# Kernel tuning notes

Measured on AMD Instinct MI355X. Metric: run time of the kernel, lower is better.

Reference implementation:

```python
import jax, jax.numpy as jnp
import numpy as np

WS = 7          # window size (square)
NUM_HEADS = 4
DIM = 128
B_ = 16384
NW = 64         # number of distinct shift masks


def _relative_coords(ws):
    # [N, N, 2] normalized relative coordinates, N = ws*ws
    ch = jnp.arange(ws, dtype=jnp.float32)
    cw = jnp.arange(ws, dtype=jnp.float32)
    coords = jnp.stack(jnp.meshgrid(ch, cw, indexing='ij'))          # [2, ws, ws]
    flat = coords.reshape(2, -1)                                      # [2, N]
    rel = flat[:, :, None] - flat[:, None, :]                         # [2, N, N]
    rel = jnp.transpose(rel, (1, 2, 0))                               # [N, N, 2]
    denom = jnp.array([max(ws - 1, 1), max(ws - 1, 1)], jnp.float32)
    return rel / denom


def setup_inputs() -> dict:
    key = jax.random.key(0)
    ks = jax.random.split(key, 8)
    N = WS * WS
    return {
        'x': jax.random.normal(ks[0], (B_, N, DIM), jnp.float32),
        'mask': jax.random.normal(ks[1], (NW, N, N), jnp.float32),
        'qkv_w': jax.random.normal(ks[2], (DIM, 3 * DIM), jnp.float32) * 0.02,
        'qkv_b': jnp.zeros((3 * DIM,), jnp.float32),
        'mlp_w1': jax.random.normal(ks[3], (2, 64), jnp.float32) * 0.5,
        'mlp_b1': jnp.zeros((64,), jnp.float32),
        'mlp_w2': jax.random.normal(ks[4], (64, NUM_HEADS), jnp.float32) * 0.1,
        'mlp_b2': jnp.zeros((NUM_HEADS,), jnp.float32),
        'proj_w': jax.random.normal(ks[5], (DIM, DIM), jnp.float32) * 0.02,
        'proj_b': jnp.zeros((DIM,), jnp.float32),
    }


def reference(x, mask, qkv_w, qkv_b, mlp_w1, mlp_b1, mlp_w2, mlp_b2, proj_w, proj_b):
    B, N, C = x.shape
    H = NUM_HEADS
    hd = C // H
    scale = hd ** (-0.5)

    qkv = (x @ qkv_w + qkv_b).reshape(B, N, 3, H, hd)
    qkv = jnp.transpose(qkv, (2, 0, 3, 1, 4))          # [3, B, H, N, hd]
    q, k, v = qkv[0] * scale, qkv[1], qkv[2]

    attn = jnp.einsum('bhnd,bhmd->bhnm', q, k)          # [B, H, N, N]

    # MLP-derived relative position bias (exact-erf GELU, as torch nn.GELU default)
    rel = _relative_coords(WS)                          # [N, N, 2]
    hmid = jax.nn.gelu(rel @ mlp_w1 + mlp_b1, approximate=False)
    bias = hmid @ mlp_w2 + mlp_b2                       # [N, N, H]
    bias = jnp.transpose(bias, (2, 0, 1))               # [H, N, N]
    attn = attn + bias[None]

    nW = mask.shape[0]
    attn = attn.reshape(B // nW, nW, H, N, N) + mask[None, :, None]
    attn = attn.reshape(B, H, N, N)
    attn = jax.nn.softmax(attn, axis=-1)

    out = jnp.einsum('bhnm,bhmd->bhnd', attn, v)        # [B, H, N, hd]
    out = jnp.transpose(out, (0, 2, 1, 3)).reshape(B, N, C)
    return out @ proj_w + proj_b
```

## Files before the change

kernel.cpp:

```cpp
#include <hip/hip_runtime.h>
#include <hip/hip_bf16.h>
#include <math.h>

typedef __bf16 bf16_t;
typedef __bf16 bf16x4 __attribute__((ext_vector_type(4)));
typedef __bf16 bf16x8 __attribute__((ext_vector_type(8)));
typedef float  f32x4  __attribute__((ext_vector_type(4)));

#define QKV_SCALE 0.17677669529663687f

#define WS_QKVWT   0u
#define WS_PROJWT  98304u
#define WS_QKVB    131072u
#define WS_BM      135168u

__global__ __launch_bounds__(256) void prep_kernel(
    const float* __restrict__ mask,
    const float* __restrict__ qkv_w, const float* __restrict__ qkv_b,
    const float* __restrict__ mlp_w1, const float* __restrict__ mlp_b1,
    const float* __restrict__ mlp_w2, const float* __restrict__ mlp_b2,
    const float* __restrict__ proj_w,
    bf16_t* __restrict__ qkv_wT, bf16_t* __restrict__ proj_wT,
    float* __restrict__ qkv_bs, float* __restrict__ bm)
{
    const int blk = blockIdx.x;
    const int tid = threadIdx.x;
    if (blk < 16) {
        const int cell = blk * 256 + tid;
        const int q = cell >> 6, kk = cell & 63;
        if (q < 49 && kk < 49) {
            const float dy = (float)(q / 7 - kk / 7) * (1.0f / 6.0f);
            const float dx = (float)(q % 7 - kk % 7) * (1.0f / 6.0f);
            float b0 = mlp_b2[0], b1 = mlp_b2[1], b2 = mlp_b2[2], b3 = mlp_b2[3];
            for (int j = 0; j < 64; ++j) {
                const float pre = dy * mlp_w1[j] + dx * mlp_w1[64 + j] + mlp_b1[j];
                const float g = 0.5f * pre * (1.0f + erff(pre * 0.70710678118654752f));
                b0 += g * mlp_w2[j * 4 + 0];
                b1 += g * mlp_w2[j * 4 + 1];
                b2 += g * mlp_w2[j * 4 + 2];
                b3 += g * mlp_w2[j * 4 + 3];
            }
            const int nm = q * 49 + kk;
            for (int wi = 0; wi < 64; ++wi) {
                const float mv = mask[wi * 2401 + nm];
                bm[(size_t)((wi * 4 + 0) << 12) + cell] = mv + b0;
                bm[(size_t)((wi * 4 + 1) << 12) + cell] = mv + b1;
                bm[(size_t)((wi * 4 + 2) << 12) + cell] = mv + b2;
                bm[(size_t)((wi * 4 + 3) << 12) + cell] = mv + b3;
            }
        } else {
            const float val = (kk >= 49) ? -3.0e38f : 0.0f;
            for (int t = 0; t < 256; ++t)
                bm[(size_t)(t << 12) + cell] = val;
        }
    } else if (blk < 208) {
        const int idx = (blk - 16) * 256 + tid;
        const int n = idx >> 7, k = idx & 127;
        float v = qkv_w[k * 384 + n];
        if (n < 128) v *= QKV_SCALE;
        qkv_wT[idx] = (bf16_t)v;
    } else if (blk < 272) {
        const int idx = (blk - 208) * 256 + tid;
        const int n = idx >> 7, k = idx & 127;
        proj_wT[idx] = (bf16_t)proj_w[k * 128 + n];
    } else {
        if (tid < 384) {
            float v = qkv_b[tid];
            if (tid < 128) v *= QKV_SCALE;
            qkv_bs[tid] = v;
        }
    }
}

__global__ __launch_bounds__(256, 3) void swin_main_kernel(
    const float* __restrict__ x,
    const bf16_t* __restrict__ qkv_wT,
    const bf16_t* __restrict__ proj_wT,
    const float* __restrict__ qkv_bs,
    const float* __restrict__ proj_b,
    const float* __restrict__ bm,
    float* __restrict__ out)
{
    __shared__ __align__(16) unsigned char smem[49152];

    const int b    = blockIdx.x;
    const int tid  = threadIdx.x;
    const int w    = tid >> 6;
    const int lane = tid & 63;
    const int c16  = lane & 15;
    const int q4   = lane >> 4;
    const int WB   = w * 12288;
    const int VB   = WB + 8192;
    const int swz  = (c16 & 7) << 4;
    const float* xg = x + (size_t)b * 6272;

    const f32x4 zf = {0.f, 0.f, 0.f, 0.f};

    f32x4 qk[4][4];
    f32x4 va[4][2];
#pragma unroll
    for (int mt = 0; mt < 4; ++mt) {
#pragma unroll
        for (int nt = 0; nt < 4; ++nt) qk[mt][nt] = zf;
        va[mt][0] = zf; va[mt][1] = zf;
    }
    const int colQK[4] = {32 * w, 32 * w + 16, 128 + 32 * w, 128 + 32 * w + 16};
    bool tv[4];
#pragma unroll
    for (int nt = 0; nt < 4; ++nt) tv[nt] = (c16 + 16 * nt) < 49;

#pragma unroll
    for (int ks = 0; ks < 4; ++ks) {
        bf16x8 xf[4];
#pragma unroll
        for (int nt = 0; nt < 4; ++nt) {
            if (tv[nt]) {
                const float* p = xg + (c16 + 16 * nt) * 128 + ks * 32 + q4 * 8;
                float4 a0 = *(const float4*)p;
                float4 a1 = *(const float4*)(p + 4);
                xf[nt][0] = (bf16_t)a0.x; xf[nt][1] = (bf16_t)a0.y;
                xf[nt][2] = (bf16_t)a0.z; xf[nt][3] = (bf16_t)a0.w;
                xf[nt][4] = (bf16_t)a1.x; xf[nt][5] = (bf16_t)a1.y;
                xf[nt][6] = (bf16_t)a1.z; xf[nt][7] = (bf16_t)a1.w;
            } else {
#pragma unroll
                for (int j = 0; j < 8; ++j) xf[nt][j] = (bf16_t)0.0f;
            }
        }
#pragma unroll
        for (int mt = 0; mt < 4; ++mt) {
            const bf16x8 wf = *(const bf16x8*)(qkv_wT + (colQK[mt] + c16) * 128 + ks * 32 + q4 * 8);
#pragma unroll
            for (int nt = 0; nt < 4; ++nt)
                qk[mt][nt] = __builtin_amdgcn_mfma_f32_16x16x32_bf16(wf, xf[nt], qk[mt][nt], 0, 0, 0);
        }
#pragma unroll
        for (int nt = 0; nt < 2; ++nt) {
            const bf16x8 vf = *(const bf16x8*)(qkv_wT + (256 + 32 * w + 16 * nt + c16) * 128 + ks * 32 + q4 * 8);
#pragma unroll
            for (int mt = 0; mt < 4; ++mt)
                va[mt][nt] = __builtin_amdgcn_mfma_f32_16x16x32_bf16(xf[mt], vf, va[mt][nt], 0, 0, 0);
        }
    }

#pragma unroll
    for (int mt = 0; mt < 4; ++mt) {
        const float4 qb = *(const float4*)(qkv_bs + colQK[mt] + 4 * q4);
        const int dim0 = (mt < 2 ? 16 * mt : 32 + 16 * (mt - 2)) + 4 * q4;
#pragma unroll
        for (int nt = 0; nt < 4; ++nt) {
            const int tok = c16 + 16 * nt;
            bf16x4 pk;
            pk[0] = (bf16_t)(qk[mt][nt][0] + qb.x);
            pk[1] = (bf16_t)(qk[mt][nt][1] + qb.y);
            pk[2] = (bf16_t)(qk[mt][nt][2] + qb.z);
            pk[3] = (bf16_t)(qk[mt][nt][3] + qb.w);
            *(bf16x4*)&smem[(WB + tok * 128 + dim0 * 2) ^ swz] = pk;
        }
    }
#pragma unroll
    for (int nt = 0; nt < 2; ++nt) {
        const float qv = qkv_bs[256 + 32 * w + 16 * nt + c16];
        const int dim = c16 + 16 * nt;
#pragma unroll
        for (int mt = 0; mt < 4; ++mt) {
            const int tok0 = 16 * mt + 4 * q4;
            bf16x4 pk;
            pk[0] = (bf16_t)(va[mt][nt][0] + qv);
            pk[1] = (bf16_t)(va[mt][nt][1] + qv);
            pk[2] = (bf16_t)(va[mt][nt][2] + qv);
            pk[3] = (bf16_t)(va[mt][nt][3] + qv);
            *(bf16x4*)&smem[(VB + dim * 128 + tok0 * 2) ^ swz] = pk;
        }
    }

    f32x4 st[4][4];
    {
        bf16x8 ka[4], qb_[4];
#pragma unroll
        for (int mt = 0; mt < 4; ++mt)
            ka[mt] = *(const bf16x8*)&smem[(WB + (c16 + 16 * mt) * 128 + 64 + 16 * q4) ^ swz];
#pragma unroll
        for (int nt = 0; nt < 4; ++nt)
            qb_[nt] = *(const bf16x8*)&smem[(WB + (c16 + 16 * nt) * 128 + 16 * q4) ^ swz];
#pragma unroll
        for (int mt = 0; mt < 4; ++mt)
#pragma unroll
            for (int nt = 0; nt < 4; ++nt)
                st[mt][nt] = __builtin_amdgcn_mfma_f32_16x16x32_bf16(ka[mt], qb_[nt], zf, 0, 0, 0),
                st[mt][nt] = st[mt][nt];
    }

    const float* bq = bm + ((size_t)(((b & 63) << 2) + w) << 12);
#pragma unroll
    for (int nt = 0; nt < 4; ++nt) {
        const int q = c16 + 16 * nt;
        float4 bv[4];
#pragma unroll
        for (int mt = 0; mt < 4; ++mt)
            bv[mt] = *(const float4*)(bq + q * 64 + 16 * mt + 4 * q4);
        float mx = -3.0e38f;
#pragma unroll
        for (int mt = 0; mt < 4; ++mt) {
            st[mt][nt][0] += bv[mt].x; st[mt][nt][1] += bv[mt].y;
            st[mt][nt][2] += bv[mt].z; st[mt][nt][3] += bv[mt].w;
#pragma unroll
            for (int r = 0; r < 4; ++r) mx = fmaxf(mx, st[mt][nt][r]);
        }
        mx = fmaxf(mx, __shfl_xor(mx, 16));
        mx = fmaxf(mx, __shfl_xor(mx, 32));
        float sm = 0.0f;
#pragma unroll
        for (int mt = 0; mt < 4; ++mt)
#pragma unroll
            for (int r = 0; r < 4; ++r) {
                const float p = __expf(st[mt][nt][r] - mx);
                st[mt][nt][r] = p;
                sm += p;
            }
        sm += __shfl_xor(sm, 16);
        sm += __shfl_xor(sm, 32);
        const float rp = 1.0f / sm;
#pragma unroll
        for (int mt = 0; mt < 4; ++mt) {
            bf16x4 pk;
#pragma unroll
            for (int r = 0; r < 4; ++r) pk[r] = (bf16_t)(st[mt][nt][r] * rp);
            *(bf16x4*)&smem[(WB + q * 128 + (16 * mt + 4 * q4) * 2) ^ swz] = pk;
        }
    }

    f32x4 ot[2][4];
#pragma unroll
    for (int mt = 0; mt < 2; ++mt)
#pragma unroll
        for (int nt = 0; nt < 4; ++nt) ot[mt][nt] = zf;
#pragma unroll
    for (int ksv = 0; ksv < 2; ++ksv) {
        bf16x8 av[2], bp[4];
#pragma unroll
        for (int mt = 0; mt < 2; ++mt)
            av[mt] = *(const bf16x8*)&smem[(VB + (c16 + 16 * mt) * 128 + 64 * ksv + 16 * q4) ^ swz];
#pragma unroll
        for (int nt = 0; nt < 4; ++nt)
            bp[nt] = *(const bf16x8*)&smem[(WB + (c16 + 16 * nt) * 128 + 64 * ksv + 16 * q4) ^ swz];
#pragma unroll
        for (int mt = 0; mt < 2; ++mt)
#pragma unroll
            for (int nt = 0; nt < 4; ++nt)
                ot[mt][nt] = __builtin_amdgcn_mfma_f32_16x16x32_bf16(av[mt], bp[nt], ot[mt][nt], 0, 0, 0);
    }

    __syncthreads();

#pragma unroll
    for (int mt = 0; mt < 2; ++mt)
#pragma unroll
        for (int nt = 0; nt < 4; ++nt) {
            const int q = c16 + 16 * nt;
            bf16x4 pk;
#pragma unroll
            for (int r = 0; r < 4; ++r) pk[r] = (bf16_t)ot[mt][nt][r];
            *(bf16x4*)&smem[(q * 256 + (32 * w + 16 * mt + 4 * q4) * 2) ^ swz] = pk;
        }
    __syncthreads();

    f32x4 pj[2][4];
#pragma unroll
    for (int mt = 0; mt < 2; ++mt)
#pragma unroll
        for (int nt = 0; nt < 4; ++nt) pj[mt][nt] = zf;
#pragma unroll
    for (int ks = 0; ks < 4; ++ks) {
        bf16x8 aw[2], bo[4];
#pragma unroll
        for (int mt = 0; mt < 2; ++mt)
            aw[mt] = *(const bf16x8*)(proj_wT + (32 * w + 16 * mt + c16) * 128 + ks * 32 + q4 * 8);
#pragma unroll
        for (int nt = 0; nt < 4; ++nt)
            bo[nt] = *(const bf16x8*)&smem[((c16 + 16 * nt) * 256 + 64 * ks + 16 * q4) ^ swz];
#pragma unroll
        for (int mt = 0; mt < 2; ++mt)
#pragma unroll
            for (int nt = 0; nt < 4; ++nt)
                pj[mt][nt] = __builtin_amdgcn_mfma_f32_16x16x32_bf16(aw[mt], bo[nt], pj[mt][nt], 0, 0, 0);
    }

    float* og = out + (size_t)b * 6272;
#pragma unroll
    for (int mt = 0; mt < 2; ++mt) {
        const int oc0 = 32 * w + 16 * mt + 4 * q4;
        const float4 pb = *(const float4*)(proj_b + oc0);
#pragma unroll
        for (int nt = 0; nt < 4; ++nt) {
            const int tok = c16 + 16 * nt;
            if (tok < 49) {
                float4 v;
                v.x = pj[mt][nt][0] + pb.x;
                v.y = pj[mt][nt][1] + pb.y;
                v.z = pj[mt][nt][2] + pb.z;
                v.w = pj[mt][nt][3] + pb.w;
                *(float4*)(og + tok * 128 + oc0) = v;
            }
        }
    }
}

extern "C" void kernel_launch(void* const* d_in, const int* in_sizes, int n_in,
                              void* d_out, int out_size, void* d_ws, size_t ws_size,
                              hipStream_t stream) {
    const float* x      = (const float*)d_in[0];
    const float* mask   = (const float*)d_in[1];
    const float* qkv_w  = (const float*)d_in[2];
    const float* qkv_b  = (const float*)d_in[3];
    const float* mlp_w1 = (const float*)d_in[4];
    const float* mlp_b1 = (const float*)d_in[5];
    const float* mlp_w2 = (const float*)d_in[6];
    const float* mlp_b2 = (const float*)d_in[7];
    const float* proj_w = (const float*)d_in[8];
    const float* proj_b = (const float*)d_in[9];
    float* out = (float*)d_out;

    unsigned char* ws = (unsigned char*)d_ws;
    bf16_t* qkv_wT  = (bf16_t*)(ws + WS_QKVWT);
    bf16_t* proj_wT = (bf16_t*)(ws + WS_PROJWT);
    float*  qkv_bs  = (float*)(ws + WS_QKVB);
    float*  bm      = (float*)(ws + WS_BM);

    hipLaunchKernelGGL(prep_kernel, dim3(273), dim3(256), 0, stream,
                       mask, qkv_w, qkv_b, mlp_w1, mlp_b1, mlp_w2, mlp_b2, proj_w,
                       qkv_wT, proj_wT, qkv_bs, bm);
    hipLaunchKernelGGL(swin_main_kernel, dim3(16384), dim3(256), 0, stream,
                       x, qkv_wT, proj_wT, qkv_bs, proj_b, bm, out);
}
```

Before: 718.6 us.

## Keep Q/K/V and softmax probabilities in registers, shrink LDS to 16KB

Q, K, V and the softmax probabilities are now repacked directly from the MFMA accumulator layout into bf16x8 operand fragments, so they no longer round-trip through shared memory. Only the per-head attention output still goes through LDS before the projection. LDS shrinks from 48KB to 16KB, and occupancy is pinned to 4 waves per EU instead of the old launch-bound hint. Projection weights are loaded with interleaved output channels so each thread writes two contiguous float4s. The V GEMM is split into a separate pass that reloads x, which adds global/L2 traffic and register pressure in exchange for removing LDS traffic.

```diff
diff --git a/kernel.cpp b/kernel.cpp
--- a/kernel.cpp
+++ b/kernel.cpp
@@ -72,7 +72,8 @@
     }
 }
 
-__global__ __launch_bounds__(256, 3) void swin_main_kernel(
+__global__ __launch_bounds__(256) __attribute__((amdgpu_waves_per_eu(4, 4)))
+void swin_main_kernel(
     const float* __restrict__ x,
     const bf16_t* __restrict__ qkv_wT,
     const bf16_t* __restrict__ proj_wT,
@@ -81,7 +82,7 @@
     const float* __restrict__ bm,
     float* __restrict__ out)
 {
-    __shared__ __align__(16) unsigned char smem[49152];
+    __shared__ __align__(16) unsigned char smem[16384];
 
     const int b    = blockIdx.x;
     const int tid  = threadIdx.x;
@@ -89,25 +90,21 @@
     const int lane = tid & 63;
     const int c16  = lane & 15;
     const int q4   = lane >> 4;
-    const int WB   = w * 12288;
-    const int VB   = WB + 8192;
     const int swz  = (c16 & 7) << 4;
     const float* xg = x + (size_t)b * 6272;
-
     const f32x4 zf = {0.f, 0.f, 0.f, 0.f};
 
+    bool tv[4];
+#pragma unroll
+    for (int nt = 0; nt < 4; ++nt) tv[nt] = (c16 + 16 * nt) < 49;
+
+    const int colQK[4] = {32 * w, 32 * w + 16, 128 + 32 * w, 128 + 32 * w + 16};
+
     f32x4 qk[4][4];
-    f32x4 va[4][2];
-#pragma unroll
-    for (int mt = 0; mt < 4; ++mt) {
+#pragma unroll
+    for (int mt = 0; mt < 4; ++mt)
 #pragma unroll
         for (int nt = 0; nt < 4; ++nt) qk[mt][nt] = zf;
-        va[mt][0] = zf; va[mt][1] = zf;
-    }
-    const int colQK[4] = {32 * w, 32 * w + 16, 128 + 32 * w, 128 + 32 * w + 16};
-    bool tv[4];
-#pragma unroll
-    for (int nt = 0; nt < 4; ++nt) tv[nt] = (c16 + 16 * nt) < 49;
 
 #pragma unroll
     for (int ks = 0; ks < 4; ++ks) {
@@ -134,67 +131,84 @@
             for (int nt = 0; nt < 4; ++nt)
                 qk[mt][nt] = __builtin_amdgcn_mfma_f32_16x16x32_bf16(wf, xf[nt], qk[mt][nt], 0, 0, 0);
         }
-#pragma unroll
-        for (int nt = 0; nt < 2; ++nt) {
-            const bf16x8 vf = *(const bf16x8*)(qkv_wT + (256 + 32 * w + 16 * nt + c16) * 128 + ks * 32 + q4 * 8);
+    }
+
+    bf16x8 Qf[4], Kf[4];
+    {
+        const float4 b0 = *(const float4*)(qkv_bs + colQK[0] + 4 * q4);
+        const float4 b1 = *(const float4*)(qkv_bs + colQK[1] + 4 * q4);
+        const float4 b2 = *(const float4*)(qkv_bs + colQK[2] + 4 * q4);
+        const float4 b3 = *(const float4*)(qkv_bs + colQK[3] + 4 * q4);
+#pragma unroll
+        for (int nt = 0; nt < 4; ++nt) {
+            Qf[nt][0] = (bf16_t)(qk[0][nt][0] + b0.x); Qf[nt][1] = (bf16_t)(qk[0][nt][1] + b0.y);
+            Qf[nt][2] = (bf16_t)(qk[0][nt][2] + b0.z); Qf[nt][3] = (bf16_t)(qk[0][nt][3] + b0.w);
+            Qf[nt][4] = (bf16_t)(qk[1][nt][0] + b1.x); Qf[nt][5] = (bf16_t)(qk[1][nt][1] + b1.y);
+            Qf[nt][6] = (bf16_t)(qk[1][nt][2] + b1.z); Qf[nt][7] = (bf16_t)(qk[1][nt][3] + b1.w);
+            Kf[nt][0] = (bf16_t)(qk[2][nt][0] + b2.x); Kf[nt][1] = (bf16_t)(qk[2][nt][1] + b2.y);
+            Kf[nt][2] = (bf16_t)(qk[2][nt][2] + b2.z); Kf[nt][3] = (bf16_t)(qk[2][nt][3] + b2.w);
+            Kf[nt][4] = (bf16_t)(qk[3][nt][0] + b3.x); Kf[nt][5] = (bf16_t)(qk[3][nt][1] + b3.y);
+            Kf[nt][6] = (bf16_t)(qk[3][nt][2] + b3.z); Kf[nt][7] = (bf16_t)(qk[3][nt][3] + b3.w);
+        }
+    }
+
+    f32x4 va[4][2];
+#pragma unroll
+    for (int mt = 0; mt < 4; ++mt) { va[mt][0] = zf; va[mt][1] = zf; }
+
+#pragma unroll
+    for (int ks = 0; ks < 4; ++ks) {
+        bf16x8 xf[4];
+#pragma unroll
+        for (int nt = 0; nt < 4; ++nt) {
+            if (tv[nt]) {
+                const float* p = xg + (c16 + 16 * nt) * 128 + ks * 32 + q4 * 8;
+                float4 a0 = *(const float4*)p;
+                float4 a1 = *(const float4*)(p + 4);
+                xf[nt][0] = (bf16_t)a0.x; xf[nt][1] = (bf16_t)a0.y;
+                xf[nt][2] = (bf16_t)a0.z; xf[nt][3] = (bf16_t)a0.w;
+                xf[nt][4] = (bf16_t)a1.x; xf[nt][5] = (bf16_t)a1.y;
+                xf[nt][6] = (bf16_t)a1.z; xf[nt][7] = (bf16_t)a1.w;
+            } else {
+#pragma unroll
+                for (int j = 0; j < 8; ++j) xf[nt][j] = (bf16_t)0.0f;
+            }
+        }
+#pragma unroll
+        for (int ntv = 0; ntv < 2; ++ntv) {
+            const bf16x8 vf = *(const bf16x8*)(qkv_wT + (256 + 32 * w + 16 * ntv + c16) * 128 + ks * 32 + q4 * 8);
 #pragma unroll
             for (int mt = 0; mt < 4; ++mt)
-                va[mt][nt] = __builtin_amdgcn_mfma_f32_16x16x32_bf16(xf[mt], vf, va[mt][nt], 0, 0, 0);
-        }
-    }
-
-#pragma unroll
-    for (int mt = 0; mt < 4; ++mt) {
-        const float4 qb = *(const float4*)(qkv_bs + colQK[mt] + 4 * q4);
-        const int dim0 = (mt < 2 ? 16 * mt : 32 + 16 * (mt - 2)) + 4 * q4;
-#pragma unroll
-        for (int nt = 0; nt < 4; ++nt) {
-            const int tok = c16 + 16 * nt;
-            bf16x4 pk;
-            pk[0] = (bf16_t)(qk[mt][nt][0] + qb.x);
-            pk[1] = (bf16_t)(qk[mt][nt][1] + qb.y);
-            pk[2] = (bf16_t)(qk[mt][nt][2] + qb.z);
-            pk[3] = (bf16_t)(qk[mt][nt][3] + qb.w);
-            *(bf16x4*)&smem[(WB + tok * 128 + dim0 * 2) ^ swz] = pk;
-        }
-    }
-#pragma unroll
-    for (int nt = 0; nt < 2; ++nt) {
-        const float qv = qkv_bs[256 + 32 * w + 16 * nt + c16];
-        const int dim = c16 + 16 * nt;
-#pragma unroll
-        for (int mt = 0; mt < 4; ++mt) {
-            const int tok0 = 16 * mt + 4 * q4;
-            bf16x4 pk;
-            pk[0] = (bf16_t)(va[mt][nt][0] + qv);
-            pk[1] = (bf16_t)(va[mt][nt][1] + qv);
-            pk[2] = (bf16_t)(va[mt][nt][2] + qv);
-            pk[3] = (bf16_t)(va[mt][nt][3] + qv);
-            *(bf16x4*)&smem[(VB + dim * 128 + tok0 * 2) ^ swz] = pk;
+                va[mt][ntv] = __builtin_amdgcn_mfma_f32_16x16x32_bf16(xf[mt], vf, va[mt][ntv], 0, 0, 0);
+        }
+    }
+
+    bf16x8 Vf[2][2];
+#pragma unroll
+    for (int ntv = 0; ntv < 2; ++ntv) {
+        const float qv = qkv_bs[256 + 32 * w + 16 * ntv + c16];
+#pragma unroll
+        for (int ksv = 0; ksv < 2; ++ksv) {
+#pragma unroll
+            for (int r = 0; r < 4; ++r) {
+                Vf[ntv][ksv][r]     = (bf16_t)(va[2 * ksv][ntv][r] + qv);
+                Vf[ntv][ksv][4 + r] = (bf16_t)(va[2 * ksv + 1][ntv][r] + qv);
+            }
         }
     }
 
     f32x4 st[4][4];
-    {
-        bf16x8 ka[4], qb_[4];
-#pragma unroll
-        for (int mt = 0; mt < 4; ++mt)
-            ka[mt] = *(const bf16x8*)&smem[(WB + (c16 + 16 * mt) * 128 + 64 + 16 * q4) ^ swz];
-#pragma unroll
-        for (int nt = 0; nt < 4; ++nt)
-            qb_[nt] = *(const bf16x8*)&smem[(WB + (c16 + 16 * nt) * 128 + 16 * q4) ^ swz];
-#pragma unroll
-        for (int mt = 0; mt < 4; ++mt)
-#pragma unroll
-            for (int nt = 0; nt < 4; ++nt)
-                st[mt][nt] = __builtin_amdgcn_mfma_f32_16x16x32_bf16(ka[mt], qb_[nt], zf, 0, 0, 0),
-                st[mt][nt] = st[mt][nt];
-    }
+#pragma unroll
+    for (int mtk = 0; mtk < 4; ++mtk)
+#pragma unroll
+        for (int ntq = 0; ntq < 4; ++ntq)
+            st[mtk][ntq] = __builtin_amdgcn_mfma_f32_16x16x32_bf16(Kf[mtk], Qf[ntq], zf, 0, 0, 0);
 
     const float* bq = bm + ((size_t)(((b & 63) << 2) + w) << 12);
-#pragma unroll
-    for (int nt = 0; nt < 4; ++nt) {
-        const int q = c16 + 16 * nt;
+    bf16x8 Pf[4][2];
+#pragma unroll
+    for (int ntq = 0; ntq < 4; ++ntq) {
+        const int q = c16 + 16 * ntq;
         float4 bv[4];
 #pragma unroll
         for (int mt = 0; mt < 4; ++mt)
@@ -202,10 +216,10 @@
         float mx = -3.0e38f;
 #pragma unroll
         for (int mt = 0; mt < 4; ++mt) {
-            st[mt][nt][0] += bv[mt].x; st[mt][nt][1] += bv[mt].y;
-            st[mt][nt][2] += bv[mt].z; st[mt][nt][3] += bv[mt].w;
-#pragma unroll
-            for (int r = 0; r < 4; ++r) mx = fmaxf(mx, st[mt][nt][r]);
+            st[mt][ntq][0] += bv[mt].x; st[mt][ntq][1] += bv[mt].y;
+            st[mt][ntq][2] += bv[mt].z; st[mt][ntq][3] += bv[mt].w;
+#pragma unroll
+            for (int r = 0; r < 4; ++r) mx = fmaxf(mx, st[mt][ntq][r]);
         }
         mx = fmaxf(mx, __shfl_xor(mx, 16));
         mx = fmaxf(mx, __shfl_xor(mx, 32));
@@ -214,94 +228,82 @@
         for (int mt = 0; mt < 4; ++mt)
 #pragma unroll
             for (int r = 0; r < 4; ++r) {
-                const float p = __expf(st[mt][nt][r] - mx);
-                st[mt][nt][r] = p;
+                const float p = __expf(st[mt][ntq][r] - mx);
+                st[mt][ntq][r] = p;
                 sm += p;
             }
         sm += __shfl_xor(sm, 16);
         sm += __shfl_xor(sm, 32);
         const float rp = 1.0f / sm;
 #pragma unroll
-        for (int mt = 0; mt < 4; ++mt) {
+        for (int ksv = 0; ksv < 2; ++ksv) {
+#pragma unroll
+            for (int r = 0; r < 4; ++r) {
+                Pf[ntq][ksv][r]     = (bf16_t)(st[2 * ksv][ntq][r] * rp);
+                Pf[ntq][ksv][4 + r] = (bf16_t)(st[2 * ksv + 1][ntq][r] * rp);
+            }
+        }
+    }
+
+    f32x4 ot[2][4];
+#pragma unroll
+    for (int ntv = 0; ntv < 2; ++ntv)
+#pragma unroll
+        for (int ntq = 0; ntq < 4; ++ntq) ot[ntv][ntq] = zf;
+#pragma unroll
+    for (int ksv = 0; ksv < 2; ++ksv)
+#pragma unroll
+        for (int ntv = 0; ntv < 2; ++ntv)
+#pragma unroll
+            for (int ntq = 0; ntq < 4; ++ntq)
+                ot[ntv][ntq] = __builtin_amdgcn_mfma_f32_16x16x32_bf16(Vf[ntv][ksv], Pf[ntq][ksv], ot[ntv][ntq], 0, 0, 0);
+
+#pragma unroll
+    for (int ntv = 0; ntv < 2; ++ntv)
+#pragma unroll
+        for (int ntq = 0; ntq < 4; ++ntq) {
+            const int tok = c16 + 16 * ntq;
             bf16x4 pk;
 #pragma unroll
-            for (int r = 0; r < 4; ++r) pk[r] = (bf16_t)(st[mt][nt][r] * rp);
-            *(bf16x4*)&smem[(WB + q * 128 + (16 * mt + 4 * q4) * 2) ^ swz] = pk;
-        }
-    }
-
-    f32x4 ot[2][4];
+            for (int r = 0; r < 4; ++r) pk[r] = (bf16_t)ot[ntv][ntq][r];
+            *(bf16x4*)&smem[(tok * 256 + (32 * w + 16 * ntv + 4 * q4) * 2) ^ swz] = pk;
+        }
+    __syncthreads();
+
+    f32x4 pj[2][4];
 #pragma unroll
     for (int mt = 0; mt < 2; ++mt)
 #pragma unroll
-        for (int nt = 0; nt < 4; ++nt) ot[mt][nt] = zf;
-#pragma unroll
-    for (int ksv = 0; ksv < 2; ++ksv) {
-        bf16x8 av[2], bp[4];
-#pragma unroll
-        for (int mt = 0; mt < 2; ++mt)
-            av[mt] = *(const bf16x8*)&smem[(VB + (c16 + 16 * mt) * 128 + 64 * ksv + 16 * q4) ^ swz];
-#pragma unroll
-        for (int nt = 0; nt < 4; ++nt)
-            bp[nt] = *(const bf16x8*)&smem[(WB + (c16 + 16 * nt) * 128 + 64 * ksv + 16 * q4) ^ swz];
-#pragma unroll
-        for (int mt = 0; mt < 2; ++mt)
-#pragma unroll
-            for (int nt = 0; nt < 4; ++nt)
-                ot[mt][nt] = __builtin_amdgcn_mfma_f32_16x16x32_bf16(av[mt], bp[nt], ot[mt][nt], 0, 0, 0);
-    }
-
-    __syncthreads();
-
-#pragma unroll
-    for (int mt = 0; mt < 2; ++mt)
-#pragma unroll
-        for (int nt = 0; nt < 4; ++nt) {
-            const int q = c16 + 16 * nt;
-            bf16x4 pk;
-#pragma unroll
-            for (int r = 0; r < 4; ++r) pk[r] = (bf16_t)ot[mt][nt][r];
-            *(bf16x4*)&smem[(q * 256 + (32 * w + 16 * mt + 4 * q4) * 2) ^ swz] = pk;
-        }
-    __syncthreads();
-
-    f32x4 pj[2][4];
-#pragma unroll
-    for (int mt = 0; mt < 2; ++mt)
-#pragma unroll
-        for (int nt = 0; nt < 4; ++nt) pj[mt][nt] = zf;
+        for (int ntq = 0; ntq < 4; ++ntq) pj[mt][ntq] = zf;
+
+    const int oc_il = 32 * w + 8 * (c16 >> 2) + (c16 & 3);
 #pragma unroll
     for (int ks = 0; ks < 4; ++ks) {
-        bf16x8 aw[2], bo[4];
-#pragma unroll
-        for (int mt = 0; mt < 2; ++mt)
-            aw[mt] = *(const bf16x8*)(proj_wT + (32 * w + 16 * mt + c16) * 128 + ks * 32 + q4 * 8);
-#pragma unroll
-        for (int nt = 0; nt < 4; ++nt)
-            bo[nt] = *(const bf16x8*)&smem[((c16 + 16 * nt) * 256 + 64 * ks + 16 * q4) ^ swz];
-#pragma unroll
-        for (int mt = 0; mt < 2; ++mt)
-#pragma unroll
-            for (int nt = 0; nt < 4; ++nt)
-                pj[mt][nt] = __builtin_amdgcn_mfma_f32_16x16x32_bf16(aw[mt], bo[nt], pj[mt][nt], 0, 0, 0);
+        const bf16x8 aw0 = *(const bf16x8*)(proj_wT + (oc_il + 0) * 128 + ks * 32 + q4 * 8);
+        const bf16x8 aw1 = *(const bf16x8*)(proj_wT + (oc_il + 4) * 128 + ks * 32 + q4 * 8);
+#pragma unroll
+        for (int ntq = 0; ntq < 4; ++ntq) {
+            const bf16x8 bo = *(const bf16x8*)&smem[((c16 + 16 * ntq) * 256 + ks * 64 + q4 * 16) ^ swz];
+            pj[0][ntq] = __builtin_amdgcn_mfma_f32_16x16x32_bf16(aw0, bo, pj[0][ntq], 0, 0, 0);
+            pj[1][ntq] = __builtin_amdgcn_mfma_f32_16x16x32_bf16(aw1, bo, pj[1][ntq], 0, 0, 0);
+        }
     }
 
     float* og = out + (size_t)b * 6272;
-#pragma unroll
-    for (int mt = 0; mt < 2; ++mt) {
-        const int oc0 = 32 * w + 16 * mt + 4 * q4;
-        const float4 pb = *(const float4*)(proj_b + oc0);
-#pragma unroll
-        for (int nt = 0; nt < 4; ++nt) {
-            const int tok = c16 + 16 * nt;
-            if (tok < 49) {
-                float4 v;
-                v.x = pj[mt][nt][0] + pb.x;
-                v.y = pj[mt][nt][1] + pb.y;
-                v.z = pj[mt][nt][2] + pb.z;
-                v.w = pj[mt][nt][3] + pb.w;
-                *(float4*)(og + tok * 128 + oc0) = v;
-            }
+    const int oc0 = 32 * w + 8 * q4;
+    const float4 pb0 = *(const float4*)(proj_b + oc0);
+    const float4 pb1 = *(const float4*)(proj_b + oc0 + 4);
+#pragma unroll
+    for (int ntq = 0; ntq < 4; ++ntq) {
+        const int tok = c16 + 16 * ntq;
+        if (tok < 49) {
+            float4 v0, v1;
+            v0.x = pj[0][ntq][0] + pb0.x; v0.y = pj[0][ntq][1] + pb0.y;
+            v0.z = pj[0][ntq][2] + pb0.z; v0.w = pj[0][ntq][3] + pb0.w;
+            v1.x = pj[1][ntq][0] + pb1.x; v1.y = pj[1][ntq][1] + pb1.y;
+            v1.z = pj[1][ntq][2] + pb1.z; v1.w = pj[1][ntq][3] + pb1.w;
+            *(float4*)(og + tok * 128 + oc0)     = v0;
+            *(float4*)(og + tok * 128 + oc0 + 4) = v1;
         }
     }
 }
```

Result: slower. 1.069 ms (+48.8%).
